# Kernel optimization log

Measured on AMD Instinct MI355X. Metric: run time of the kernel, lower is better.

The kernel has to match this reference:

```python
import jax, jax.numpy as jnp
import numpy as np

N, D, H = 8192, 512, 512

def setup_inputs() -> dict:
    key = jax.random.key(0)
    ks = jax.random.split(key, 9)
    s_in = 1.0 / np.sqrt(D)
    s_h = 1.0 / np.sqrt(H)
    return {
        "x": jax.random.normal(ks[0], (N, D), jnp.float32),
        "Wq": jax.random.uniform(ks[1], (D, H), jnp.float32, -s_in, s_in),
        "bq": jax.random.uniform(ks[2], (H,), jnp.float32, -s_in, s_in),
        "Wk": jax.random.uniform(ks[3], (D, H), jnp.float32, -s_in, s_in),
        "bk": jax.random.uniform(ks[4], (H,), jnp.float32, -s_in, s_in),
        "Wv": jax.random.uniform(ks[5], (D, H), jnp.float32, -s_in, s_in),
        "bv": jax.random.uniform(ks[6], (H,), jnp.float32, -s_in, s_in),
        "Wo": jax.random.uniform(ks[7], (H, H), jnp.float32, -s_h, s_h),
        "bo": jax.random.uniform(ks[8], (H,), jnp.float32, -s_h, s_h),
    }

def reference(x, Wq, bq, Wk, bk, Wv, bv, Wo, bo):
    q = x @ Wq + bq            # [N, H]
    k = x @ Wk + bk            # [N, H]
    v = x @ Wv + bv            # [N, H]
    scores = (q @ k.T) * (1.0 / jnp.sqrt(jnp.asarray(H, q.dtype)))  # [N, N]
    attn = jax.nn.softmax(scores, axis=-1)
    attended = attn @ v        # [N, H]
    return attended @ Wo + bo  # [N, H]
```

## Files before the change

kernel.cpp:

```cpp
#include <hip/hip_runtime.h>

typedef short sh8 __attribute__((ext_vector_type(8)));
typedef float f32x4 __attribute__((ext_vector_type(4)));

#define DEV __device__ __forceinline__

DEV f32x4 mfma16(sh8 a, sh8 b, f32x4 c) {
  return __builtin_amdgcn_mfma_f32_16x16x32_bf16(a, b, c, 0, 0, 0);
}

DEV unsigned short f2bf(float f) {
  unsigned u = __float_as_uint(f);
  u = u + 0x7FFFu + ((u >> 16) & 1u);
  return (unsigned short)(u >> 16);
}

DEV unsigned cvtpk(float lo, float hi) {
  unsigned r;
  asm("v_cvt_pk_bf16_f32 %0, %1, %2" : "=v"(r) : "v"(lo), "v"(hi));
  return r;
}

DEV void gll16(const void* g, void* l) {
  __builtin_amdgcn_global_load_lds(
      (const __attribute__((address_space(1))) unsigned int*)g,
      (__attribute__((address_space(3))) unsigned int*)l, 16, 0, 0);
}

__global__ void cvt_x_kernel(const float* __restrict__ x, unsigned short* __restrict__ xb, int n4) {
  int i = blockIdx.x * blockDim.x + threadIdx.x;
  int stride = gridDim.x * blockDim.x;
  for (; i < n4; i += stride) {
    float4 v = ((const float4*)x)[i];
    ushort4 o;
    o.x = f2bf(v.x); o.y = f2bf(v.y); o.z = f2bf(v.z); o.w = f2bf(v.w);
    ((ushort4*)xb)[i] = o;
  }
}

__global__ void cvt_wT_kernel(const float* __restrict__ W0, const float* __restrict__ W1,
                              const float* __restrict__ W2, const float* __restrict__ W3,
                              unsigned short* __restrict__ T0, unsigned short* __restrict__ T1,
                              unsigned short* __restrict__ T2, unsigned short* __restrict__ T3) {
  const float* W; unsigned short* T;
  switch (blockIdx.z) {
    case 0: W = W0; T = T0; break;
    case 1: W = W1; T = T1; break;
    case 2: W = W2; T = T2; break;
    default: W = W3; T = T3; break;
  }
  __shared__ float tile[32][33];
  int tx = threadIdx.x & 31, ty = threadIdx.x >> 5;
  int r0 = blockIdx.y * 32, c0 = blockIdx.x * 32;
#pragma unroll
  for (int i = 0; i < 4; i++) tile[ty + i * 8][tx] = W[(r0 + ty + i * 8) * 512 + c0 + tx];
  __syncthreads();
#pragma unroll
  for (int i = 0; i < 4; i++) T[(c0 + ty + i * 8) * 512 + r0 + tx] = f2bf(tile[tx][ty + i * 8]);
}

__global__ __launch_bounds__(512, 2) void gemm256_u_kernel(
    const unsigned short* __restrict__ Q, const unsigned short* __restrict__ Kb,
    unsigned short* __restrict__ U, float* __restrict__ lpart) {
  __shared__ __align__(16) unsigned short smem[65536];
  const int tid = threadIdx.x, lane = tid & 63;
  const int w = tid >> 6;
  const int g = lane >> 4, r = lane & 15;
  const int wm2 = w & 1, wn4 = w >> 1;
  const int xcd = blockIdx.x & 7, j = blockIdx.x >> 3;
  const int brow = ((xcd & 1) * 16 + (j & 15)) * 256;
  const int bcol = ((xcd >> 1) * 8 + (j >> 4)) * 256;
  const int srow = tid >> 3;
  const int sg = tid & 7;

  f32x4 acc[2][2][4][2] = {};

#define STG(b, a, h, kt)                                                                       \
  do {                                                                                         \
    const unsigned short* _src = (a) ? Kb : Q;                                                 \
    int _base = (a) ? bcol : brow;                                                             \
    int _r0 = (h) * 128 + srow;                                                                \
    int _r1 = _r0 + 64;                                                                        \
    unsigned short* _d = smem + (b) * 32768 + (a) * 16384 + (h) * 8192 + tid * 8;              \
    gll16(_src + (size_t)(_base + _r0) * 512 + (kt) * 64 + ((sg ^ (_r0 & 7)) * 8), _d);        \
    gll16(_src + (size_t)(_base + _r1) * 512 + (kt) * 64 + ((sg ^ (_r1 & 7)) * 8), _d + 4096); \
  } while (0)

  auto LDK = [&](sh8 (&kf)[2][4], int B_, int kh) {
    const unsigned short* Bs = smem + B_ * 32768 + 16384;
#pragma unroll
    for (int kk = 0; kk < 2; kk++)
#pragma unroll
      for (int m = 0; m < 4; m++) {
        int row = kh * 128 + wm2 * 64 + m * 16 + r;
        kf[kk][m] = *(const sh8*)&Bs[row * 64 + (((kk * 4 + g) ^ (r & 7)) * 8)];
      }
  };
  auto LDQ = [&](sh8 (&qf)[2][2], int B_, int qh) {
    const unsigned short* As = smem + B_ * 32768;
#pragma unroll
    for (int kk = 0; kk < 2; kk++)
#pragma unroll
      for (int n = 0; n < 2; n++) {
        int row = qh * 128 + wn4 * 32 + n * 16 + r;
        qf[kk][n] = *(const sh8*)&As[row * 64 + (((kk * 4 + g) ^ (r & 7)) * 8)];
      }
  };
  auto MM = [&](f32x4 (&c)[4][2], sh8 (&kf)[2][4], sh8 (&qf)[2][2]) {
    __builtin_amdgcn_s_setprio(1);
#pragma unroll
    for (int kk = 0; kk < 2; kk++)
#pragma unroll
      for (int m = 0; m < 4; m++)
#pragma unroll
        for (int n = 0; n < 2; n++)
          c[m][n] = mfma16(kf[kk][m], qf[kk][n], c[m][n]);
    __builtin_amdgcn_s_setprio(0);
  };
#define BAR asm volatile("s_barrier" ::: "memory")
#define VM2 asm volatile("s_waitcnt vmcnt(2)" ::: "memory")

  STG(0, 0, 0, 0); STG(0, 0, 1, 0); STG(0, 1, 0, 0); STG(0, 1, 1, 0);
  asm volatile("s_waitcnt vmcnt(0)" ::: "memory");
  BAR;

#pragma unroll
  for (int kt = 0; kt < 8; ++kt) {
    const int cur = kt & 1, nb = cur ^ 1;
    const int kn = (kt < 7) ? kt + 1 : 7;
    sh8 k0[2][4], k1[2][4], q0[2][2], q1[2][2];
    LDK(k0, cur, 0); LDQ(q0, cur, 0);
    STG(nb, 0, 0, kn);
    VM2; BAR;
    MM(acc[0][0], k0, q0);
    LDQ(q1, cur, 1);
    STG(nb, 0, 1, kn);
    BAR;
    MM(acc[0][1], k0, q1);
    LDK(k1, cur, 1);
    STG(nb, 1, 0, kn);
    BAR;
    MM(acc[1][0], k1, q0);
    STG(nb, 1, 1, kn);
    VM2; BAR;
    MM(acc[1][1], k1, q1);
  }
#undef STG

  asm volatile("s_waitcnt vmcnt(0)" ::: "memory");
  __syncthreads();

  const float K2c = 0.04419417382415922f * 1.4426950408889634f;
#pragma unroll
  for (int qh = 0; qh < 2; qh++)
#pragma unroll
    for (int n = 0; n < 2; n++) {
      int qr = qh * 128 + wn4 * 32 + n * 16 + r;
      float s = 0.f;
#pragma unroll
      for (int kh = 0; kh < 2; kh++)
#pragma unroll
        for (int m = 0; m < 4; m++) {
          f32x4 a = acc[kh][qh][m][n];
          float v0 = __builtin_amdgcn_exp2f(a[0] * K2c);
          float v1 = __builtin_amdgcn_exp2f(a[1] * K2c);
          float v2 = __builtin_amdgcn_exp2f(a[2] * K2c);
          float v3 = __builtin_amdgcn_exp2f(a[3] * K2c);
          s += (v0 + v1) + (v2 + v3);
          uint2 pk; pk.x = cvtpk(v0, v1); pk.y = cvtpk(v2, v3);
          int ke = kh * 128 + wm2 * 64 + m * 16 + g * 4;
          int el = qr * 256 + (ke ^ ((qr & 7) * 8));
          *(uint2*)&smem[el] = pk;
        }
      s += __shfl_xor(s, 16);
      s += __shfl_xor(s, 32);
      if (g == 0)
        lpart[(size_t)((bcol >> 7) + wm2) * 8192 + brow + qr] = s;
    }
  __syncthreads();
#pragma unroll
  for (int jj = 0; jj < 16; jj++) {
    int row = jj * 16 + (tid >> 5);
    int g32 = tid & 31;
    uint4 v = *(const uint4*)&smem[row * 256 + ((g32 ^ (row & 7)) * 8)];
    *(uint4*)&U[(size_t)(brow + row) * 8192 + bcol + g32 * 8] = v;
  }
}

__global__ __launch_bounds__(512, 2) void gemm256_pv_kernel(
    const unsigned short* __restrict__ Uu, const unsigned short* __restrict__ VT,
    unsigned short* __restrict__ P0, unsigned short* __restrict__ P1,
    unsigned short* __restrict__ P2, unsigned short* __restrict__ P3) {
  __shared__ __align__(16) unsigned short smem[65536];
  const int tid = threadIdx.x, lane = tid & 63;
  const int w = tid >> 6;
  const int g = lane >> 4, r = lane & 15;
  const int wm2 = w & 1, wn4 = w >> 1;
  const int c = blockIdx.x & 7;
  const int hi = blockIdx.x >> 3;
  const int nt = hi & 1, qthi = hi >> 1;
  const int qlo = c >> 2, kz = c & 3;
  const int qt = qthi * 2 + qlo;
  const int brow = qt * 256;
  const int bcol = nt * 256;
  const int koff = kz * 2048;
  const int srow = tid >> 3;
  const int sg = tid & 7;
  unsigned short* P = (kz == 0) ? P0 : (kz == 1) ? P1 : (kz == 2) ? P2 : P3;

  f32x4 acc[2][2][4][2] = {};

#define STGP(b, a, h, kt)                                                                        \
  do {                                                                                           \
    const unsigned short* _src = (a) ? VT : Uu;                                                  \
    int _base = (a) ? bcol : brow;                                                               \
    int _r0 = (h) * 128 + srow;                                                                  \
    int _r1 = _r0 + 64;                                                                          \
    unsigned short* _d = smem + (b) * 32768 + (a) * 16384 + (h) * 8192 + tid * 8;                \
    gll16(_src + (size_t)(_base + _r0) * 8192 + koff + (kt) * 64 + ((sg ^ (_r0 & 7)) * 8), _d);  \
    gll16(_src + (size_t)(_base + _r1) * 8192 + koff + (kt) * 64 + ((sg ^ (_r1 & 7)) * 8),       \
          _d + 4096);                                                                            \
  } while (0)

  auto LDV = [&](sh8 (&vf)[2][4], int B_, int dh) {
    const unsigned short* Bs = smem + B_ * 32768 + 16384;
#pragma unroll
    for (int kk = 0; kk < 2; kk++)
#pragma unroll
      for (int m = 0; m < 4; m++) {
        int row = dh * 128 + wm2 * 64 + m * 16 + r;
        vf[kk][m] = *(const sh8*)&Bs[row * 64 + (((kk * 4 + g) ^ (r & 7)) * 8)];
      }
  };
  auto LDU = [&](sh8 (&uf)[2][2], int B_, int qh) {
    const unsigned short* As = smem + B_ * 32768;
#pragma unroll
    for (int kk = 0; kk < 2; kk++)
#pragma unroll
      for (int n = 0; n < 2; n++) {
        int row = qh * 128 + wn4 * 32 + n * 16 + r;
        uf[kk][n] = *(const sh8*)&As[row * 64 + (((kk * 4 + g) ^ (r & 7)) * 8)];
      }
  };
  auto MM = [&](f32x4 (&cc)[4][2], sh8 (&vf)[2][4], sh8 (&uf)[2][2]) {
    __builtin_amdgcn_s_setprio(1);
#pragma unroll
    for (int kk = 0; kk < 2; kk++)
#pragma unroll
      for (int m = 0; m < 4; m++)
#pragma unroll
        for (int n = 0; n < 2; n++)
          cc[m][n] = mfma16(vf[kk][m], uf[kk][n], cc[m][n]);
    __builtin_amdgcn_s_setprio(0);
  };

  STGP(0, 0, 0, 0); STGP(0, 0, 1, 0); STGP(0, 1, 0, 0); STGP(0, 1, 1, 0);
  asm volatile("s_waitcnt vmcnt(0)" ::: "memory");
  BAR;

#pragma unroll 2
  for (int kt = 0; kt < 32; ++kt) {
    const int cur = kt & 1, nb = cur ^ 1;
    const int kn = (kt < 31) ? kt + 1 : 31;
    sh8 v0[2][4], v1[2][4], u0[2][2], u1[2][2];
    LDV(v0, cur, 0); LDU(u0, cur, 0);
    STGP(nb, 0, 0, kn);
    VM2; BAR;
    MM(acc[0][0], v0, u0);
    LDU(u1, cur, 1);
    STGP(nb, 0, 1, kn);
    BAR;
    MM(acc[0][1], v0, u1);
    LDV(v1, cur, 1);
    STGP(nb, 1, 0, kn);
    BAR;
    MM(acc[1][0], v1, u0);
    STGP(nb, 1, 1, kn);
    VM2; BAR;
    MM(acc[1][1], v1, u1);
  }
#undef STGP
#undef BAR
#undef VM2

  asm volatile("s_waitcnt vmcnt(0)" ::: "memory");
  __syncthreads();

#pragma unroll
  for (int qh = 0; qh < 2; qh++)
#pragma unroll
    for (int n = 0; n < 2; n++) {
      int qr = qh * 128 + wn4 * 32 + n * 16 + r;
#pragma unroll
      for (int dh = 0; dh < 2; dh++)
#pragma unroll
        for (int m = 0; m < 4; m++) {
          f32x4 a = acc[dh][qh][m][n];
          uint2 pk; pk.x = cvtpk(a[0], a[1]); pk.y = cvtpk(a[2], a[3]);
          int de = dh * 128 + wm2 * 64 + m * 16 + g * 4;
          int el = qr * 256 + (de ^ ((qr & 7) * 8));
          *(uint2*)&smem[el] = pk;
        }
    }
  __syncthreads();
#pragma unroll
  for (int jj = 0; jj < 16; jj++) {
    int row = jj * 16 + (tid >> 5);
    int g32 = tid & 31;
    uint4 v = *(const uint4*)&smem[row * 256 + ((g32 ^ (row & 7)) * 8)];
    *(uint4*)&P[(size_t)(brow + row) * 512 + bcol + g32 * 8] = v;
  }
}

template <int MODE>
DEV void gemm_core(const unsigned short* __restrict__ A, int lda,
                   const unsigned short* __restrict__ Bt, int ldb,
                   const float* __restrict__ bias, void* __restrict__ Cv, int ldc,
                   int kSteps, int koff, int brow, int bcol,
                   unsigned short* smem) {
  const int tid = threadIdx.x, lane = tid & 63, w = tid >> 6;
  const int g = lane >> 4, r = lane & 15;
  const int wr = w >> 1, wc = w & 1;
  const int rA = w * 8 + (lane >> 3);
  const int sgl = lane & 7;
  const int scol = ((sgl ^ (lane >> 3)) * 8);
  const unsigned short* aP = A + (size_t)(brow + rA) * lda + koff + scol;
  const unsigned short* bP = Bt + (size_t)(bcol + rA) * ldb + koff + scol;
  const int lOff = rA * 64 + sgl * 8;
  f32x4 acc[4][4] = {};
  const int fr = r & 7;

  auto STAGE = [&](int buf, int ks) {
    unsigned short* lA = smem + buf * 16384 + lOff;
    unsigned short* lB = smem + buf * 16384 + 8192 + lOff;
    const size_t ko = (size_t)ks * 64;
#pragma unroll
    for (int cc = 0; cc < 4; cc++) gll16(aP + (size_t)cc * 32 * lda + ko, lA + cc * 32 * 64);
#pragma unroll
    for (int cc = 0; cc < 4; cc++) gll16(bP + (size_t)cc * 32 * ldb + ko, lB + cc * 32 * 64);
  };
  auto COMPUTE = [&](int buf) {
    const unsigned short* As = smem + buf * 16384;
    const unsigned short* Bs = As + 8192;
#pragma unroll
    for (int kk = 0; kk < 2; kk++) {
      sh8 af[4], bfr[4];
#pragma unroll
      for (int m = 0; m < 4; m++)
        af[m] = *(const sh8*)&As[(wr * 64 + m * 16 + r) * 64 + (((kk * 4 + g) ^ fr) * 8)];
#pragma unroll
      for (int n = 0; n < 4; n++)
        bfr[n] = *(const sh8*)&Bs[(wc * 64 + n * 16 + r) * 64 + (((kk * 4 + g) ^ fr) * 8)];
#pragma unroll
      for (int m = 0; m < 4; m++)
#pragma unroll
        for (int n = 0; n < 4; n++) acc[m][n] = mfma16(af[m], bfr[n], acc[m][n]);
    }
  };

  STAGE(0, 0);
  int cur = 0;
  for (int ks = 0; ks + 1 < kSteps; ks++) {
    STAGE(cur ^ 1, ks + 1);
    asm volatile("s_waitcnt vmcnt(8)" ::: "memory");
    asm volatile("s_barrier" ::: "memory");
    COMPUTE(cur);
    asm volatile("s_barrier" ::: "memory");
    cur ^= 1;
  }
  asm volatile("s_waitcnt vmcnt(0)" ::: "memory");
  asm volatile("s_barrier" ::: "memory");
  COMPUTE(cur);

  if (MODE == 0) {
#pragma unroll
    for (int n = 0; n < 4; n++) {
      int col = bcol + wc * 64 + n * 16 + r;
      float bv = bias ? bias[col] : 0.f;
#pragma unroll
      for (int m = 0; m < 4; m++) {
        int row = brow + wr * 64 + m * 16 + g * 4;
#pragma unroll
        for (int i = 0; i < 4; i++)
          ((float*)Cv)[(size_t)(row + i) * ldc + col] = acc[m][n][i] + bv;
      }
    }
  } else {
    __syncthreads();
#pragma unroll
    for (int m = 0; m < 4; m++) {
#pragma unroll
      for (int n = 0; n < 4; n++) {
        int coll = wc * 64 + n * 16 + r;
        float bv = bias ? bias[bcol + coll] : 0.f;
        int rb = (wr * 64 + m * 16 + g * 4) * 132 + coll;
        smem[rb] = f2bf(acc[m][n][0] + bv);
        smem[rb + 132] = f2bf(acc[m][n][1] + bv);
        smem[rb + 264] = f2bf(acc[m][n][2] + bv);
        smem[rb + 396] = f2bf(acc[m][n][3] + bv);
      }
    }
    __syncthreads();
    unsigned short* C = (unsigned short*)Cv;
#pragma unroll
    for (int j = 0; j < 8; j++) {
      int row = w * 32 + j * 4 + (lane >> 4);
      int colb = (lane & 15) * 8;
      uint4 v = *(const uint4*)&smem[row * 132 + colb];
      *(uint4*)&C[(size_t)(brow + row) * ldc + bcol + colb] = v;
    }
  }
}

__global__ __launch_bounds__(256, 2) void gemm_qkv_kernel(
    const unsigned short* __restrict__ A,
    const unsigned short* __restrict__ B0, const unsigned short* __restrict__ B1,
    const unsigned short* __restrict__ B2,
    const float* __restrict__ c0, const float* __restrict__ c1, const float* __restrict__ c2,
    unsigned short* __restrict__ C0, unsigned short* __restrict__ C1,
    unsigned short* __restrict__ C2) {
  __shared__ __align__(16) unsigned short smem[32768];
  const unsigned short* Bt; const float* bias; unsigned short* C;
  switch (blockIdx.z) {
    case 0: Bt = B0; bias = c0; C = C0; break;
    case 1: Bt = B1; bias = c1; C = C1; break;
    default: Bt = B2; bias = c2; C = C2; break;
  }
  gemm_core<1>(A, 512, Bt, 512, bias, C, 512, 8, 0,
               blockIdx.x * 128, blockIdx.y * 128, smem);
}

__global__ __launch_bounds__(256, 2) void gemm_o_kernel(
    const unsigned short* __restrict__ att, const unsigned short* __restrict__ woT,
    const float* __restrict__ bo, float* __restrict__ out) {
  __shared__ __align__(16) unsigned short smem[32768];
  gemm_core<0>(att, 512, woT, 512, bo, out, 512, 8, 0,
               blockIdx.x * 128, blockIdx.y * 128, smem);
}

__global__ void transpose_v_kernel(const unsigned short* __restrict__ in, unsigned short* __restrict__ out) {
  __shared__ unsigned short tile[32][33];
  int tx = threadIdx.x & 31, ty = threadIdx.x >> 5;
  int r0 = blockIdx.y * 32, c0 = blockIdx.x * 32;
#pragma unroll
  for (int i = 0; i < 4; i++) tile[ty + i * 8][tx] = in[(size_t)(r0 + ty + i * 8) * 512 + c0 + tx];
  __syncthreads();
#pragma unroll
  for (int i = 0; i < 4; i++) out[(size_t)(c0 + ty + i * 8) * 8192 + r0 + tx] = tile[tx][ty + i * 8];
}

__global__ void combine_l_kernel(const float* __restrict__ lpart, float* __restrict__ linv) {
  int row = blockIdx.x * 256 + threadIdx.x;
  float s = 0.f;
#pragma unroll 8
  for (int j = 0; j < 64; j++) s += lpart[(size_t)j * 8192 + row];
  linv[row] = 1.0f / s;
}

__global__ void addcvt4_kernel(const unsigned short* __restrict__ p0,
                               const unsigned short* __restrict__ p1,
                               const unsigned short* __restrict__ p2,
                               const unsigned short* __restrict__ p3,
                               const float* __restrict__ linv,
                               unsigned short* __restrict__ o, int n8) {
  int i = blockIdx.x * blockDim.x + threadIdx.x;
  int stride = gridDim.x * blockDim.x;
  for (; i < n8; i += stride) {
    float inv = linv[i >> 6];
    uint4 a = ((const uint4*)p0)[i];
    uint4 b = ((const uint4*)p1)[i];
    uint4 c = ((const uint4*)p2)[i];
    uint4 d = ((const uint4*)p3)[i];
    const unsigned* ua = (const unsigned*)&a;
    const unsigned* ub = (const unsigned*)&b;
    const unsigned* uc = (const unsigned*)&c;
    const unsigned* ud = (const unsigned*)&d;
    unsigned out[4];
#pragma unroll
    for (int e = 0; e < 4; e++) {
      float lo = __uint_as_float(ua[e] << 16) + __uint_as_float(ub[e] << 16) +
                 __uint_as_float(uc[e] << 16) + __uint_as_float(ud[e] << 16);
      float hi = __uint_as_float(ua[e] & 0xffff0000u) + __uint_as_float(ub[e] & 0xffff0000u) +
                 __uint_as_float(uc[e] & 0xffff0000u) + __uint_as_float(ud[e] & 0xffff0000u);
      out[e] = cvtpk(lo * inv, hi * inv);
    }
    ((uint4*)o)[i] = *(uint4*)out;
  }
}

extern "C" void kernel_launch(void* const* d_in, const int* in_sizes, int n_in,
                              void* d_out, int out_size, void* d_ws, size_t ws_size,
                              hipStream_t stream) {
  const float* x  = (const float*)d_in[0];
  const float* Wq = (const float*)d_in[1];
  const float* bq = (const float*)d_in[2];
  const float* Wk = (const float*)d_in[3];
  const float* bk = (const float*)d_in[4];
  const float* Wv = (const float*)d_in[5];
  const float* bv = (const float*)d_in[6];
  const float* Wo = (const float*)d_in[7];
  const float* bo = (const float*)d_in[8];
  char* ws = (char*)d_ws;

  unsigned short* U   = (unsigned short*)(ws + 0);
  unsigned short* xb  = (unsigned short*)(ws + 0);
  unsigned short* vb  = (unsigned short*)(ws + 8388608);
  unsigned short* att = (unsigned short*)(ws + 0);
  unsigned short* qb  = (unsigned short*)(ws + 134217728);
  unsigned short* kb  = (unsigned short*)(ws + 142606336);
  unsigned short* vtb = (unsigned short*)(ws + 150994944);
  unsigned short* wqT = (unsigned short*)(ws + 159383552);
  unsigned short* wkT = (unsigned short*)(ws + 159907840);
  unsigned short* wvT = (unsigned short*)(ws + 160432128);
  unsigned short* woT = (unsigned short*)(ws + 160956416);
  float* lpart = (float*)(ws + 161480704);
  float* linv  = (float*)(ws + 165675008);
  unsigned short* P0 = qb;
  unsigned short* P1 = kb;
  unsigned short* P2 = (unsigned short*)d_out;
  unsigned short* P3 = (unsigned short*)d_out + 4194304;

  cvt_x_kernel<<<2048, 256, 0, stream>>>(x, xb, 8192 * 512 / 4);
  cvt_wT_kernel<<<dim3(16, 16, 4), 256, 0, stream>>>(Wq, Wk, Wv, Wo, wqT, wkT, wvT, woT);
  gemm_qkv_kernel<<<dim3(64, 4, 3), 256, 0, stream>>>(
      xb, wqT, wkT, wvT, bq, bk, bv, qb, kb, vb);
  transpose_v_kernel<<<dim3(16, 256), 256, 0, stream>>>(vb, vtb);
  gemm256_u_kernel<<<1024, 512, 0, stream>>>(qb, kb, U, lpart);
  combine_l_kernel<<<32, 256, 0, stream>>>(lpart, linv);
  gemm256_pv_kernel<<<256, 512, 0, stream>>>(U, vtb, P0, P1, P2, P3);
  addcvt4_kernel<<<2048, 256, 0, stream>>>(P0, P1, P2, P3, linv, att, 8192 * 512 / 8);
  gemm_o_kernel<<<dim3(64, 4), 256, 0, stream>>>(att, woT, bo, (float*)d_out);
}
```

Baseline: 204.8 us.

## Fuse V transpose into QKV GEMM epilogue and prefetch first K/V fragments

The V projection now writes its output already transposed through shared memory inside the QKV GEMM epilogue, which removes the separate transpose kernel and its extra global round trip. Separately, the U and PV GEMM main loops load the first K/V LDS fragment of the next iteration early, so LDS reads overlap the last MFMA group. This uses more registers, and the transposed epilogue writes shorter contiguous runs to a buffer with an 8192-element stride.

```diff
diff --git a/kernel.cpp b/kernel.cpp
--- a/kernel.cpp
+++ b/kernel.cpp
@@ -124,12 +124,15 @@
   asm volatile("s_waitcnt vmcnt(0)" ::: "memory");
   BAR;
 
+  sh8 k0[2][4];
+  LDK(k0, 0, 0);
+
 #pragma unroll
   for (int kt = 0; kt < 8; ++kt) {
     const int cur = kt & 1, nb = cur ^ 1;
     const int kn = (kt < 7) ? kt + 1 : 7;
-    sh8 k0[2][4], k1[2][4], q0[2][2], q1[2][2];
-    LDK(k0, cur, 0); LDQ(q0, cur, 0);
+    sh8 k1[2][4], q0[2][2], q1[2][2];
+    LDQ(q0, cur, 0);
     STG(nb, 0, 0, kn);
     VM2; BAR;
     MM(acc[0][0], k0, q0);
@@ -143,6 +146,7 @@
     MM(acc[1][0], k1, q0);
     STG(nb, 1, 1, kn);
     VM2; BAR;
+    if (kt < 7) LDK(k0, nb, 0);
     MM(acc[1][1], k1, q1);
   }
 #undef STG
@@ -258,12 +262,15 @@
   asm volatile("s_waitcnt vmcnt(0)" ::: "memory");
   BAR;
 
+  sh8 v0[2][4];
+  LDV(v0, 0, 0);
+
 #pragma unroll 2
   for (int kt = 0; kt < 32; ++kt) {
     const int cur = kt & 1, nb = cur ^ 1;
     const int kn = (kt < 31) ? kt + 1 : 31;
-    sh8 v0[2][4], v1[2][4], u0[2][2], u1[2][2];
-    LDV(v0, cur, 0); LDU(u0, cur, 0);
+    sh8 v1[2][4], u0[2][2], u1[2][2];
+    LDU(u0, cur, 0);
     STGP(nb, 0, 0, kn);
     VM2; BAR;
     MM(acc[0][0], v0, u0);
@@ -277,6 +284,7 @@
     MM(acc[1][0], v1, u0);
     STGP(nb, 1, 1, kn);
     VM2; BAR;
+    if (kt < 31) LDV(v0, nb, 0);
     MM(acc[1][1], v1, u1);
   }
 #undef STGP
@@ -317,7 +325,7 @@
                    const unsigned short* __restrict__ Bt, int ldb,
                    const float* __restrict__ bias, void* __restrict__ Cv, int ldc,
                    int kSteps, int koff, int brow, int bcol,
-                   unsigned short* smem) {
+                   unsigned short* smem, bool transp) {
   const int tid = threadIdx.x, lane = tid & 63, w = tid >> 6;
   const int g = lane >> 4, r = lane & 15;
   const int wr = w >> 1, wc = w & 1;
@@ -387,27 +395,52 @@
     }
   } else {
     __syncthreads();
-#pragma unroll
-    for (int m = 0; m < 4; m++) {
-#pragma unroll
-      for (int n = 0; n < 4; n++) {
-        int coll = wc * 64 + n * 16 + r;
-        float bv = bias ? bias[bcol + coll] : 0.f;
-        int rb = (wr * 64 + m * 16 + g * 4) * 132 + coll;
-        smem[rb] = f2bf(acc[m][n][0] + bv);
-        smem[rb + 132] = f2bf(acc[m][n][1] + bv);
-        smem[rb + 264] = f2bf(acc[m][n][2] + bv);
-        smem[rb + 396] = f2bf(acc[m][n][3] + bv);
-      }
-    }
-    __syncthreads();
-    unsigned short* C = (unsigned short*)Cv;
-#pragma unroll
-    for (int j = 0; j < 8; j++) {
-      int row = w * 32 + j * 4 + (lane >> 4);
-      int colb = (lane & 15) * 8;
-      uint4 v = *(const uint4*)&smem[row * 132 + colb];
-      *(uint4*)&C[(size_t)(brow + row) * ldc + bcol + colb] = v;
+    if (!transp) {
+#pragma unroll
+      for (int m = 0; m < 4; m++) {
+#pragma unroll
+        for (int n = 0; n < 4; n++) {
+          int coll = wc * 64 + n * 16 + r;
+          float bv = bias ? bias[bcol + coll] : 0.f;
+          int rb = (wr * 64 + m * 16 + g * 4) * 132 + coll;
+          smem[rb] = f2bf(acc[m][n][0] + bv);
+          smem[rb + 132] = f2bf(acc[m][n][1] + bv);
+          smem[rb + 264] = f2bf(acc[m][n][2] + bv);
+          smem[rb + 396] = f2bf(acc[m][n][3] + bv);
+        }
+      }
+      __syncthreads();
+      unsigned short* C = (unsigned short*)Cv;
+#pragma unroll
+      for (int jj = 0; jj < 8; jj++) {
+        int row = w * 32 + jj * 4 + (lane >> 4);
+        int colb = (lane & 15) * 8;
+        uint4 v = *(const uint4*)&smem[row * 132 + colb];
+        *(uint4*)&C[(size_t)(brow + row) * ldc + bcol + colb] = v;
+      }
+    } else {
+#pragma unroll
+      for (int m = 0; m < 4; m++) {
+#pragma unroll
+        for (int n = 0; n < 4; n++) {
+          int coll = wc * 64 + n * 16 + r;
+          float bv = bias ? bias[bcol + coll] : 0.f;
+          int qrow = wr * 64 + m * 16 + g * 4;
+          uint2 pk;
+          pk.x = cvtpk(acc[m][n][0] + bv, acc[m][n][1] + bv);
+          pk.y = cvtpk(acc[m][n][2] + bv, acc[m][n][3] + bv);
+          *(uint2*)&smem[coll * 132 + qrow] = pk;
+        }
+      }
+      __syncthreads();
+      unsigned short* C = (unsigned short*)Cv;
+#pragma unroll
+      for (int jj = 0; jj < 8; jj++) {
+        int hrow = w * 32 + jj * 4 + (lane >> 4);
+        int nb8 = (lane & 15) * 8;
+        uint4 v = *(const uint4*)&smem[hrow * 132 + nb8];
+        *(uint4*)&C[(size_t)(bcol + hrow) * ldc + brow + nb8] = v;
+      }
     }
   }
 }
@@ -418,16 +451,17 @@
     const unsigned short* __restrict__ B2,
     const float* __restrict__ c0, const float* __restrict__ c1, const float* __restrict__ c2,
     unsigned short* __restrict__ C0, unsigned short* __restrict__ C1,
-    unsigned short* __restrict__ C2) {
+    unsigned short* __restrict__ CT2) {
   __shared__ __align__(16) unsigned short smem[32768];
   const unsigned short* Bt; const float* bias; unsigned short* C;
+  bool tr; int ldc;
   switch (blockIdx.z) {
-    case 0: Bt = B0; bias = c0; C = C0; break;
-    case 1: Bt = B1; bias = c1; C = C1; break;
-    default: Bt = B2; bias = c2; C = C2; break;
-  }
-  gemm_core<1>(A, 512, Bt, 512, bias, C, 512, 8, 0,
-               blockIdx.x * 128, blockIdx.y * 128, smem);
+    case 0: Bt = B0; bias = c0; C = C0; tr = false; ldc = 512; break;
+    case 1: Bt = B1; bias = c1; C = C1; tr = false; ldc = 512; break;
+    default: Bt = B2; bias = c2; C = CT2; tr = true; ldc = 8192; break;
+  }
+  gemm_core<1>(A, 512, Bt, 512, bias, C, ldc, 8, 0,
+               blockIdx.x * 128, blockIdx.y * 128, smem, tr);
 }
 
 __global__ __launch_bounds__(256, 2) void gemm_o_kernel(
@@ -435,18 +469,7 @@
     const float* __restrict__ bo, float* __restrict__ out) {
   __shared__ __align__(16) unsigned short smem[32768];
   gemm_core<0>(att, 512, woT, 512, bo, out, 512, 8, 0,
-               blockIdx.x * 128, blockIdx.y * 128, smem);
-}
-
-__global__ void transpose_v_kernel(const unsigned short* __restrict__ in, unsigned short* __restrict__ out) {
-  __shared__ unsigned short tile[32][33];
-  int tx = threadIdx.x & 31, ty = threadIdx.x >> 5;
-  int r0 = blockIdx.y * 32, c0 = blockIdx.x * 32;
-#pragma unroll
-  for (int i = 0; i < 4; i++) tile[ty + i * 8][tx] = in[(size_t)(r0 + ty + i * 8) * 512 + c0 + tx];
-  __syncthreads();
-#pragma unroll
-  for (int i = 0; i < 4; i++) out[(size_t)(c0 + ty + i * 8) * 8192 + r0 + tx] = tile[tx][ty + i * 8];
+               blockIdx.x * 128, blockIdx.y * 128, smem, false);
 }
 
 __global__ void combine_l_kernel(const float* __restrict__ lpart, float* __restrict__ linv) {
@@ -504,7 +527,6 @@
 
   unsigned short* U   = (unsigned short*)(ws + 0);
   unsigned short* xb  = (unsigned short*)(ws + 0);
-  unsigned short* vb  = (unsigned short*)(ws + 8388608);
   unsigned short* att = (unsigned short*)(ws + 0);
   unsigned short* qb  = (unsigned short*)(ws + 134217728);
   unsigned short* kb  = (unsigned short*)(ws + 142606336);
@@ -523,8 +545,7 @@
   cvt_x_kernel<<<2048, 256, 0, stream>>>(x, xb, 8192 * 512 / 4);
   cvt_wT_kernel<<<dim3(16, 16, 4), 256, 0, stream>>>(Wq, Wk, Wv, Wo, wqT, wkT, wvT, woT);
   gemm_qkv_kernel<<<dim3(64, 4, 3), 256, 0, stream>>>(
-      xb, wqT, wkT, wvT, bq, bk, bv, qb, kb, vb);
-  transpose_v_kernel<<<dim3(16, 256), 256, 0, stream>>>(vb, vtb);
+      xb, wqT, wkT, wvT, bq, bk, bv, qb, kb, vtb);
   gemm256_u_kernel<<<1024, 512, 0, stream>>>(qb, kb, U, lpart);
   combine_l_kernel<<<32, 256, 0, stream>>>(lpart, linv);
   gemm256_pv_kernel<<<256, 512, 0, stream>>>(U, vtb, P0, P1, P2, P3);
```

New measurement: 291.9 us. +42.5%, slower.
